# Kernel optimization log

Hardware: AMD Instinct MI355X
Metric: run time of the kernel (lower is better)

The kernel has to match this reference:

```python
import jax, jax.numpy as jnp
import numpy as np

FILTER_FACTOR = 10  # init kwarg


def median_filter2d(x, k, padding="REFLECT", constant_values=0.0):
    """Faithful port of tfa.image.median_filter2d for NHWC float input.

    tfa pads with pad_top=(k-1)//2, pad_bottom=k-1-pad_top (same for width),
    extracts k*k patches per pixel/channel, and takes the element that
    tf.nn.top_k(patches, area//2+1)[..., -1] yields, i.e. the value at
    ascending-sorted index (area-1)//2.
    """
    B, H, W, C = x.shape
    pt = (k - 1) // 2
    pb = k - 1 - pt
    mode = {"REFLECT": "reflect", "SYMMETRIC": "symmetric", "CONSTANT": "constant"}[padding]
    if mode == "constant":
        xp = jnp.pad(x, ((0, 0), (pt, pb), (pt, pb), (0, 0)), mode=mode,
                     constant_values=constant_values)
    else:
        xp = jnp.pad(x, ((0, 0), (pt, pb), (pt, pb), (0, 0)), mode=mode)
    # Gather sliding windows via advanced indexing (vectorized, no data loops).
    ih = jnp.arange(H)[:, None] + jnp.arange(k)[None, :]  # (H, k)
    iw = jnp.arange(W)[:, None] + jnp.arange(k)[None, :]  # (W, k)
    rows = xp[:, ih]                 # (B, H, k, Wp, C)
    patches = rows[:, :, :, iw]      # (B, H, k, W, k, C)
    patches = patches.transpose(0, 1, 3, 5, 2, 4).reshape(B, H, W, C, k * k)
    area = k * k
    med = jnp.sort(patches, axis=-1)[..., (area - 1) // 2]  # (B, H, W, C)
    return med


def setup_inputs() -> dict:
    key = jax.random.key(0)
    k1, k2 = jax.random.split(key)
    inputs = jax.random.uniform(k1, (2, 224, 224, 3), dtype=jnp.float32)
    # layer draws blend ~ U[0.1, 1.0)
    blend = jax.random.uniform(k2, (1,), dtype=jnp.float32) * 0.9 + 0.1
    return {"inputs": inputs, "blend": blend}


def reference(inputs, blend):
    # training=True path: median filter then tfa.image.blend(filtered, inputs, blend)
    # blend(image1, image2, f) = image1 + f * (image2 - image1)
    k = inputs.shape[1] // FILTER_FACTOR  # height // filter_factor
    filt = median_filter2d(inputs, k, padding="REFLECT", constant_values=0.0)
    f = blend[0]
    return filt + f * (inputs - filt)
```

## Files before the change

### kernel.cpp

```cpp
#include <hip/hip_runtime.h>


#define HH 224
#define WW 224
#define CHN 3
#define KK 22
#define PT 10
#define AREA (KK * KK)
#define RANK 242
#define PXW 8
#define XGS (WW / PXW)
#define DT 2

#define INFF  __int_as_float(0x7f800000)
#define NINFF __int_as_float(0xff800000)

__device__ __forceinline__ int reflect224(int g) {
    int a = abs(g);
    return min(a, 2 * (HH - 1) - a);
}

__device__ __forceinline__ int count8(const float v[8], float t) {
    int c = 0;
#pragma unroll
    for (int i = 0; i < 8; ++i)
        c += __popcll(__ballot(v[i] < t));
    return c;
}

__device__ __forceinline__ float tree8(const float v[8]) {
    return fmaxf(fmaxf(fmaxf(v[0], v[1]), fmaxf(v[2], v[3])),
                 fmaxf(fmaxf(v[4], v[5]), fmaxf(v[6], v[7])));
}

__device__ __forceinline__ float half_bfly(float m) {
    m = fmaxf(m, __int_as_float(__builtin_amdgcn_ds_swizzle(__float_as_int(m), 0x401F)));
    m = fmaxf(m, __int_as_float(__builtin_amdgcn_ds_swizzle(__float_as_int(m), 0x201F)));
    m = fmaxf(m, __int_as_float(__builtin_amdgcn_ds_swizzle(__float_as_int(m), 0x101F)));
    m = fmaxf(m, __int_as_float(__builtin_amdgcn_ds_swizzle(__float_as_int(m), 0x081F)));
    m = fmaxf(m, __int_as_float(__builtin_amdgcn_ds_swizzle(__float_as_int(m), 0x041F)));
    return m;
}

__device__ __forceinline__ float bperm32(float x, int axor32) {
    return __int_as_float(
        __builtin_amdgcn_ds_bpermute(axor32, __float_as_int(x)));
}

__device__ __forceinline__ void gather(float v[8], const float* __restrict__ img,
                                       const int voff[8], int lane, int x) {
    if (x >= PT && x <= WW - 1 - (KK - 1 - PT)) {
        const float* base = img + (x - PT) * CHN;
#pragma unroll
        for (int i = 0; i < 8; ++i) v[i] = base[voff[i]];
    } else {
#pragma unroll
        for (int i = 0; i < 8; ++i) {
            int s   = i * 64 + lane;
            int se  = min(s, AREA - 1);
            int row = se / KK;
            int col = se - row * KK;
            int gy672 = voff[i] - col * CHN;
            int gx = reflect224(x - PT + col);
            v[i] = img[gy672 + gx * CHN];
        }
    }
    v[7] = (lane < AREA - 448) ? v[7] : INFF;
}

__global__ __launch_bounds__(256)
void median_blend_kernel(const float* __restrict__ in,
                         const float* __restrict__ blend,
                         float* __restrict__ out) {
    const int lane = threadIdx.x & 63;
    const int wid  = threadIdx.x >> 6;
    const int wg = blockIdx.x * 4 + wid;
    const int xg = wg % XGS;
    const int t1 = wg / XGS;
    const int y  = t1 % HH;
    const int t2 = t1 / HH;
    const int c  = t2 % CHN;
    const int b  = t2 / CHN;

    const float f = blend[0];
    const float* img  = in  + (size_t)b * (HH * WW * CHN) + c;
    float*       outp = out + (size_t)b * (HH * WW * CHN) + c;

    int voff[8];
#pragma unroll
    for (int i = 0; i < 8; ++i) {
        int s   = i * 64 + lane;
        int se  = min(s, AREA - 1);
        int row = se / KK;
        int col = se - row * KK;
        int gy  = reflect224(y - PT + row);
        voff[i] = gy * (WW * CHN) + col * CHN;
    }

    const int axor32 = (lane ^ 32) << 2;
    const float ninf = NINFF;
    const float NINV = -1.0f / (float)AREA;

    const int x0 = xg * PXW;
    float tprev = 0.5f;

#pragma unroll 1
    for (int j = 0; j < PXW; j += 2) {
        const int xA = x0 + j;
        const int xB = xA + 1;

        float vA[8], vB[8];
        gather(vA, img, voff, lane, xA);
        gather(vB, img, voff, lane, xB);

        float tA = tprev, tB = tprev;
        int CA = count8(vA, tA);
        int CB = count8(vB, tB);
        int dA = CA - RANK, dB = CB - RANK;
        float loA = 0.0f, hiA = 1.0f, loB = 0.0f, hiB = 1.0f;
        bool actA = (dA > DT || dA < -DT), actB = (dB > DT || dB < -DT);
#pragma unroll 1
        for (int it = 0; it < 20 && (actA || actB); ++it) {
            if (actA) {
                if (dA > 0) hiA = tA; else loA = tA;
                float tn = fmaf((float)dA, NINV, tA);
                if (!(tn > loA && tn < hiA)) tn = 0.5f * (loA + hiA);
                if (!(tn > loA && tn < hiA)) actA = false;
                else {
                    tA = tn;
                    CA = count8(vA, tA);
                    dA = CA - RANK;
                    actA = (dA > DT || dA < -DT);
                }
            }
            if (actB) {
                if (dB > 0) hiB = tB; else loB = tB;
                float tn = fmaf((float)dB, NINV, tB);
                if (!(tn > loB && tn < hiB)) tn = 0.5f * (loB + hiB);
                if (!(tn > loB && tn < hiB)) actB = false;
                else {
                    tB = tn;
                    CB = count8(vB, tB);
                    dB = CB - RANK;
                    actB = (dB > DT || dB < -DT);
                }
            }
        }

        const bool topA = (dA >= 0), topB = (dB >= 0);
        int eA = topA ? dA + 1 : -dA;
        int eB = topB ? dB + 1 : -dB;
        const int sgnA = topA ? 0 : (int)0x80000000;
        const int sgnB = topB ? 0 : (int)0x80000000;
        if (topA) {
#pragma unroll
            for (int i = 0; i < 8; ++i) vA[i] = (vA[i] < tA) ? vA[i] : ninf;
        } else {
#pragma unroll
            for (int i = 0; i < 8; ++i) vA[i] = (vA[i] < tA) ? ninf : -vA[i];
        }
        if (topB) {
#pragma unroll
            for (int i = 0; i < 8; ++i) vB[i] = (vB[i] < tB) ? vB[i] : ninf;
        } else {
#pragma unroll
            for (int i = 0; i < 8; ++i) vB[i] = (vB[i] < tB) ? ninf : -vB[i];
        }

        float medA = tA, medB = tB;
        bool doneA = false, doneB = false;
#pragma unroll 1
        for (int r = 0; r < 300 && !(doneA && doneB); ++r) {
            float pA = doneA ? ninf : tree8(vA);
            float pB = doneB ? ninf : tree8(vB);
            pA = fmaxf(pA, bperm32(pA, axor32));
            pB = fmaxf(pB, bperm32(pB, axor32));
            float m = (lane < 32) ? pA : pB;
            m = half_bfly(m);
            const float mA = __int_as_float(
                __builtin_amdgcn_readlane(__float_as_int(m), 0));
            const float mB = __int_as_float(
                __builtin_amdgcn_readlane(__float_as_int(m), 32));
            if (!doneA) {
                int q = 0;
#pragma unroll
                for (int i = 0; i < 8; ++i)
                    q += __popcll(__ballot(vA[i] == mA));
                if (eA <= q) {
                    medA = __int_as_float(__float_as_int(mA) ^ sgnA);
                    doneA = true;
                } else {
                    eA -= q;
#pragma unroll
                    for (int i = 0; i < 8; ++i)
                        vA[i] = (vA[i] == mA) ? ninf : vA[i];
                }
            }
            if (!doneB) {
                int q = 0;
#pragma unroll
                for (int i = 0; i < 8; ++i)
                    q += __popcll(__ballot(vB[i] == mB));
                if (eB <= q) {
                    medB = __int_as_float(__float_as_int(mB) ^ sgnB);
                    doneB = true;
                } else {
                    eB -= q;
#pragma unroll
                    for (int i = 0; i < 8; ++i)
                        vB[i] = (vB[i] == mB) ? ninf : vB[i];
                }
            }
        }
        tprev = medB;

        const float xcA = img[y * (WW * CHN) + xA * CHN];
        const float xcB = img[y * (WW * CHN) + xB * CHN];
        if (lane == 0) {
            outp[y * (WW * CHN) + xA * CHN] = medA + f * (xcA - medA);
            outp[y * (WW * CHN) + xB * CHN] = medB + f * (xcB - medB);
        }
    }
}

extern "C" void kernel_launch(void* const* d_in, const int* in_sizes, int n_in,
                              void* d_out, int out_size, void* d_ws, size_t ws_size,
                              hipStream_t stream) {
    const float* in    = (const float*)d_in[0];
    const float* blend = (const float*)d_in[1];
    float* out = (float*)d_out;

    const int nwaves  = 2 * CHN * HH * XGS;
    const int nblocks = nwaves / 4;
    median_blend_kernel<<<nblocks, 256, 0, stream>>>(in, blend, out);
}
```

Measured before the change: 153.6 us.

## Use persistent waves with atomic work counter and drop threshold bracketing

```diff
diff --git a/kernel.cpp b/kernel.cpp
--- a/kernel.cpp
+++ b/kernel.cpp
@@ -11,6 +11,7 @@
 #define PXW 8
 #define XGS (WW / PXW)
 #define DT 2
+#define NGROUPS (2 * CHN * HH * XGS)
 
 #define INFF  __int_as_float(0x7f800000)
 #define NINFF __int_as_float(0xff800000)
@@ -71,154 +72,150 @@
 __global__ __launch_bounds__(256)
 void median_blend_kernel(const float* __restrict__ in,
                          const float* __restrict__ blend,
-                         float* __restrict__ out) {
+                         float* __restrict__ out,
+                         int* __restrict__ ctr) {
     const int lane = threadIdx.x & 63;
-    const int wid  = threadIdx.x >> 6;
-    const int wg = blockIdx.x * 4 + wid;
-    const int xg = wg % XGS;
-    const int t1 = wg / XGS;
-    const int y  = t1 % HH;
-    const int t2 = t1 / HH;
-    const int c  = t2 % CHN;
-    const int b  = t2 / CHN;
 
     const float f = blend[0];
-    const float* img  = in  + (size_t)b * (HH * WW * CHN) + c;
-    float*       outp = out + (size_t)b * (HH * WW * CHN) + c;
-
-    int voff[8];
-#pragma unroll
-    for (int i = 0; i < 8; ++i) {
-        int s   = i * 64 + lane;
-        int se  = min(s, AREA - 1);
-        int row = se / KK;
-        int col = se - row * KK;
-        int gy  = reflect224(y - PT + row);
-        voff[i] = gy * (WW * CHN) + col * CHN;
-    }
-
     const int axor32 = (lane ^ 32) << 2;
     const float ninf = NINFF;
     const float NINV = -1.0f / (float)AREA;
 
-    const int x0 = xg * PXW;
     float tprev = 0.5f;
 
 #pragma unroll 1
-    for (int j = 0; j < PXW; j += 2) {
-        const int xA = x0 + j;
-        const int xB = xA + 1;
-
-        float vA[8], vB[8];
-        gather(vA, img, voff, lane, xA);
-        gather(vB, img, voff, lane, xB);
-
-        float tA = tprev, tB = tprev;
-        int CA = count8(vA, tA);
-        int CB = count8(vB, tB);
-        int dA = CA - RANK, dB = CB - RANK;
-        float loA = 0.0f, hiA = 1.0f, loB = 0.0f, hiB = 1.0f;
-        bool actA = (dA > DT || dA < -DT), actB = (dB > DT || dB < -DT);
-#pragma unroll 1
-        for (int it = 0; it < 20 && (actA || actB); ++it) {
-            if (actA) {
-                if (dA > 0) hiA = tA; else loA = tA;
-                float tn = fmaf((float)dA, NINV, tA);
-                if (!(tn > loA && tn < hiA)) tn = 0.5f * (loA + hiA);
-                if (!(tn > loA && tn < hiA)) actA = false;
-                else {
-                    tA = tn;
+    for (;;) {
+        int wgv = 0;
+        if (lane == 0) wgv = atomicAdd(ctr, 1);
+        const int wg = __builtin_amdgcn_readfirstlane(wgv);
+        if (wg >= NGROUPS) break;
+
+        const int xg = wg % XGS;
+        const int t1 = wg / XGS;
+        const int y  = t1 % HH;
+        const int t2 = t1 / HH;
+        const int c  = t2 % CHN;
+        const int b  = t2 / CHN;
+
+        const float* img  = in  + (size_t)b * (HH * WW * CHN) + c;
+        float*       outp = out + (size_t)b * (HH * WW * CHN) + c;
+
+        int voff[8];
+#pragma unroll
+        for (int i = 0; i < 8; ++i) {
+            int s   = i * 64 + lane;
+            int se  = min(s, AREA - 1);
+            int row = se / KK;
+            int col = se - row * KK;
+            int gy  = reflect224(y - PT + row);
+            voff[i] = gy * (WW * CHN) + col * CHN;
+        }
+
+        const int x0 = xg * PXW;
+
+#pragma unroll 1
+        for (int j = 0; j < PXW; j += 2) {
+            const int xA = x0 + j;
+            const int xB = xA + 1;
+
+            float vA[8], vB[8];
+            gather(vA, img, voff, lane, xA);
+            gather(vB, img, voff, lane, xB);
+
+            float tA = tprev, tB = tprev;
+            int CA = count8(vA, tA);
+            int CB = count8(vB, tB);
+            int dA = CA - RANK, dB = CB - RANK;
+            bool actA = (dA > DT || dA < -DT), actB = (dB > DT || dB < -DT);
+#pragma unroll 1
+            for (int it = 0; it < 12 && (actA || actB); ++it) {
+                if (actA) {
+                    tA = fmaf((float)dA, NINV, tA);
                     CA = count8(vA, tA);
                     dA = CA - RANK;
                     actA = (dA > DT || dA < -DT);
                 }
-            }
-            if (actB) {
-                if (dB > 0) hiB = tB; else loB = tB;
-                float tn = fmaf((float)dB, NINV, tB);
-                if (!(tn > loB && tn < hiB)) tn = 0.5f * (loB + hiB);
-                if (!(tn > loB && tn < hiB)) actB = false;
-                else {
-                    tB = tn;
+                if (actB) {
+                    tB = fmaf((float)dB, NINV, tB);
                     CB = count8(vB, tB);
                     dB = CB - RANK;
                     actB = (dB > DT || dB < -DT);
                 }
             }
-        }
-
-        const bool topA = (dA >= 0), topB = (dB >= 0);
-        int eA = topA ? dA + 1 : -dA;
-        int eB = topB ? dB + 1 : -dB;
-        const int sgnA = topA ? 0 : (int)0x80000000;
-        const int sgnB = topB ? 0 : (int)0x80000000;
-        if (topA) {
-#pragma unroll
-            for (int i = 0; i < 8; ++i) vA[i] = (vA[i] < tA) ? vA[i] : ninf;
-        } else {
-#pragma unroll
-            for (int i = 0; i < 8; ++i) vA[i] = (vA[i] < tA) ? ninf : -vA[i];
-        }
-        if (topB) {
-#pragma unroll
-            for (int i = 0; i < 8; ++i) vB[i] = (vB[i] < tB) ? vB[i] : ninf;
-        } else {
-#pragma unroll
-            for (int i = 0; i < 8; ++i) vB[i] = (vB[i] < tB) ? ninf : -vB[i];
-        }
-
-        float medA = tA, medB = tB;
-        bool doneA = false, doneB = false;
-#pragma unroll 1
-        for (int r = 0; r < 300 && !(doneA && doneB); ++r) {
-            float pA = doneA ? ninf : tree8(vA);
-            float pB = doneB ? ninf : tree8(vB);
-            pA = fmaxf(pA, bperm32(pA, axor32));
-            pB = fmaxf(pB, bperm32(pB, axor32));
-            float m = (lane < 32) ? pA : pB;
-            m = half_bfly(m);
-            const float mA = __int_as_float(
-                __builtin_amdgcn_readlane(__float_as_int(m), 0));
-            const float mB = __int_as_float(
-                __builtin_amdgcn_readlane(__float_as_int(m), 32));
-            if (!doneA) {
-                int q = 0;
-#pragma unroll
-                for (int i = 0; i < 8; ++i)
-                    q += __popcll(__ballot(vA[i] == mA));
-                if (eA <= q) {
-                    medA = __int_as_float(__float_as_int(mA) ^ sgnA);
-                    doneA = true;
-                } else {
-                    eA -= q;
+
+            const bool topA = (dA >= 0), topB = (dB >= 0);
+            int eA = topA ? dA + 1 : -dA;
+            int eB = topB ? dB + 1 : -dB;
+            const int sgnA = topA ? 0 : (int)0x80000000;
+            const int sgnB = topB ? 0 : (int)0x80000000;
+            if (topA) {
+#pragma unroll
+                for (int i = 0; i < 8; ++i) vA[i] = (vA[i] < tA) ? vA[i] : ninf;
+            } else {
+#pragma unroll
+                for (int i = 0; i < 8; ++i) vA[i] = (vA[i] < tA) ? ninf : -vA[i];
+            }
+            if (topB) {
+#pragma unroll
+                for (int i = 0; i < 8; ++i) vB[i] = (vB[i] < tB) ? vB[i] : ninf;
+            } else {
+#pragma unroll
+                for (int i = 0; i < 8; ++i) vB[i] = (vB[i] < tB) ? ninf : -vB[i];
+            }
+
+            float medA = tA, medB = tB;
+            bool doneA = false, doneB = false;
+#pragma unroll 1
+            for (int r = 0; r < 300 && !(doneA && doneB); ++r) {
+                float pA = doneA ? ninf : tree8(vA);
+                float pB = doneB ? ninf : tree8(vB);
+                pA = fmaxf(pA, bperm32(pA, axor32));
+                pB = fmaxf(pB, bperm32(pB, axor32));
+                float m = (lane < 32) ? pA : pB;
+                m = half_bfly(m);
+                const float mA = __int_as_float(
+                    __builtin_amdgcn_readlane(__float_as_int(m), 0));
+                const float mB = __int_as_float(
+                    __builtin_amdgcn_readlane(__float_as_int(m), 32));
+                if (!doneA) {
+                    int q = 0;
 #pragma unroll
                     for (int i = 0; i < 8; ++i)
-                        vA[i] = (vA[i] == mA) ? ninf : vA[i];
-                }
-            }
-            if (!doneB) {
-                int q = 0;
-#pragma unroll
-                for (int i = 0; i < 8; ++i)
-                    q += __popcll(__ballot(vB[i] == mB));
-                if (eB <= q) {
-                    medB = __int_as_float(__float_as_int(mB) ^ sgnB);
-                    doneB = true;
-                } else {
-                    eB -= q;
+                        q += __popcll(__ballot(vA[i] == mA));
+                    if (eA <= q) {
+                        medA = __int_as_float(__float_as_int(mA) ^ sgnA);
+                        doneA = true;
+                    } else {
+                        eA -= q;
+#pragma unroll
+                        for (int i = 0; i < 8; ++i)
+                            vA[i] = (vA[i] == mA) ? ninf : vA[i];
+                    }
+                }
+                if (!doneB) {
+                    int q = 0;
 #pragma unroll
                     for (int i = 0; i < 8; ++i)
-                        vB[i] = (vB[i] == mB) ? ninf : vB[i];
-                }
-            }
-        }
-        tprev = medB;
-
-        const float xcA = img[y * (WW * CHN) + xA * CHN];
-        const float xcB = img[y * (WW * CHN) + xB * CHN];
-        if (lane == 0) {
-            outp[y * (WW * CHN) + xA * CHN] = medA + f * (xcA - medA);
-            outp[y * (WW * CHN) + xB * CHN] = medB + f * (xcB - medB);
+                        q += __popcll(__ballot(vB[i] == mB));
+                    if (eB <= q) {
+                        medB = __int_as_float(__float_as_int(mB) ^ sgnB);
+                        doneB = true;
+                    } else {
+                        eB -= q;
+#pragma unroll
+                        for (int i = 0; i < 8; ++i)
+                            vB[i] = (vB[i] == mB) ? ninf : vB[i];
+                    }
+                }
+            }
+            tprev = medB;
+
+            const float xcA = img[y * (WW * CHN) + xA * CHN];
+            const float xcB = img[y * (WW * CHN) + xB * CHN];
+            if (lane == 0) {
+                outp[y * (WW * CHN) + xA * CHN] = medA + f * (xcA - medA);
+                outp[y * (WW * CHN) + xB * CHN] = medB + f * (xcB - medB);
+            }
         }
     }
 }
@@ -229,8 +226,10 @@
     const float* in    = (const float*)d_in[0];
     const float* blend = (const float*)d_in[1];
     float* out = (float*)d_out;
-
-    const int nwaves  = 2 * CHN * HH * XGS;
-    const int nblocks = nwaves / 4;
-    median_blend_kernel<<<nblocks, 256, 0, stream>>>(in, blend, out);
-}
+    int*   ctr = (int*)d_ws;
+
+    hipMemsetAsync(ctr, 0, sizeof(int), stream);
+
+    const int nblocks = 2048;
+    median_blend_kernel<<<nblocks, 256, 0, stream>>>(in, blend, out, ctr);
+}
```

After: 590.0 us. +284.0%, slower.
